# Kernel optimization log

Measured on AMD Instinct MI355X. Metric: run time of the kernel, lower is better.

The kernel has to match this reference:

```python
import jax, jax.numpy as jnp
import numpy as np

N, E, C, EMB, NB, L = 20000, 640000, 64, 32, 8, 2
MAX_RADIUS = 2.5
NUM_NEIGHBORS = 32.0
RH = 32  # radial MLP hidden


def setup_inputs() -> dict:
    key = jax.random.key(0)
    ks = jax.random.split(key, 24)
    g = lambda k, shape, fan: (jax.random.normal(k, shape, dtype=jnp.float32) / np.sqrt(fan).astype(np.float32))
    inp = {
        'x': jax.random.normal(ks[0], (N, 6), dtype=jnp.float32),
        'batch': jnp.zeros((N,), dtype=jnp.int64),
        'node_attr': jax.random.randint(ks[1], (N,), 0, 100),
        'edge_src': jax.random.randint(ks[2], (E,), 0, N),
        'edge_dst': jax.random.randint(ks[3], (E,), 0, N),
        'emb_table': jax.random.normal(ks[4], (100, EMB), dtype=jnp.float32),
        'uplift_M': jax.random.normal(ks[5], (C, 2), dtype=jnp.float32),
        'h': jnp.ones((L,), jnp.float32) * 0.01,
        'mix': jnp.ones((L,), jnp.float32) * 0.5,
        'rad_W1': g(ks[6], (L, NB, RH), NB),
        'rad_b1': jnp.zeros((L, RH), jnp.float32),
        'rad_W2': g(ks[7], (L, RH, 2 * C), RH),
        'lin1_s': g(ks[8], (L, C, C), C),
        'lin1_v': g(ks[9], (L, C, C), C),
        'lin2_s': g(ks[10], (L, C, 2 * C), C),
        'lin2_v': g(ks[11], (L, C, C), C),
        'sc_s_w': g(ks[12], (L, C, EMB, 2 * C), C * EMB),
        'sc_v_w': g(ks[13], (L, C, EMB, C), C * EMB),
        'si_s': g(ks[14], (L, C, C), C),
        'si_v': g(ks[15], (L, C, C), C),
    }
    return inp


def _forward(x, batch, node_attr, edge_src, edge_dst, emb_table, uplift_M, h, mix,
             rad_W1, rad_b1, rad_W2, lin1_s, lin1_v, lin2_s, lin2_v,
             sc_s_w, sc_v_w, si_s, si_v):
    n = x.shape[0]
    emb = emb_table[node_attr]                       # [N, EMB] node embedding
    # semi-unitarize uplift matrix: Q = M (M^T M)^{-1/2} == U V^T
    U, _, Vt = jnp.linalg.svd(uplift_M, full_matrices=False)
    Q = U @ Vt                                       # [C, 2]
    xv = x.reshape(n, 2, 3)
    y_s = jnp.zeros((n, C), x.dtype)                 # hidden scalars start at 0
    y_v = jnp.einsum('nkx,ck->ncx', xv, Q)           # uplift vectors [N,C,3]
    y = (y_s, y_v)
    y_old = y
    nbas = jnp.arange(1, NB + 1, dtype=x.dtype)
    inv_nn = 1.0 / np.sqrt(NUM_NEIGHBORS).astype(np.float32)
    for i in range(L):
        pos = x[:, :3]
        ev = pos[edge_src] - pos[edge_dst]           # [E,3]
        elen = jnp.linalg.norm(ev, axis=1)
        safe = jnp.maximum(elen, 1e-9)
        sh = np.float32(np.sqrt(3.0)) * ev / safe[:, None]   # 1x1o SH, component norm
        # bessel radial basis, scaled by sqrt(NB)
        ef = (np.float32(np.sqrt(2.0 / MAX_RADIUS)) *
              jnp.sin(nbas[None, :] * jnp.pi * safe[:, None] / MAX_RADIUS) / safe[:, None])
        ef = ef * np.float32(np.sqrt(NB))
        # smooth cutoff (e3nn tetris style)
        u = 2.0 * (elen / MAX_RADIUS - 1.0)
        cut = jnp.where(u > 0, 0.0, jnp.where(u < -2, 1.0, 0.5 * (1.0 - jnp.cos(jnp.pi * u))))
        ea = cut[:, None] * sh                       # [E,3] edge attr
        # linear pre-mix
        s1 = y[0] @ lin1_s[i]                        # [N,C]
        v1 = jnp.einsum('ncx,cd->ndx', y[1], lin1_v[i])  # [N,C,3]
        # radial MLP -> per-edge TP weights
        w = jax.nn.silu(ef @ rad_W1[i] + rad_b1[i]) @ rad_W2[i]  # [E,2C]
        w1, w2 = w[:, :C], w[:, C:]
        # tensor-product messages: 0e x 1o -> 1o ; 1o . 1o -> 0e
        msg_v = (w1 * s1[edge_src])[:, :, None] * ea[:, None, :]        # [E,C,3]
        msg_s = w2 * jnp.einsum('ecx,ex->ec', v1[edge_src], ea)         # [E,C]
        agg_s = jax.ops.segment_sum(msg_s, edge_dst, num_segments=n) * inv_nn
        agg_v = jax.ops.segment_sum(msg_v, edge_dst, num_segments=n) * inv_nn
        # post linear + node-attr self connection
        out_s = agg_s @ lin2_s[i] + jnp.einsum('nc,ne,ceo->no', y[0], emb, sc_s_w[i])   # [N,2C]
        out_v = (jnp.einsum('ncx,cd->ndx', agg_v, lin2_v[i]) +
                 jnp.einsum('ncx,ne,ceo->nox', y[1], emb, sc_v_w[i]))                   # [N,C,3]
        # gated nonlinearity
        g_s = jax.nn.silu(out_s[:, :C])
        g_v = jax.nn.sigmoid(out_s[:, C:])[:, :, None] * out_v
        # self interaction
        y2_s = y[0] @ si_s[i]
        y2_v = jnp.einsum('ncx,cd->ndx', y[1], si_v[i])
        # leapfrog update
        hh = h[i] * h[i]
        m = mix[i]
        new_s = 2.0 * y[0] - y_old[0] + hh * (m * g_s + (m - 1.0) * y2_s)
        new_v = 2.0 * y[1] - y_old[1] + hh * (m * g_v + (m - 1.0) * y2_v)
        y_old = y
        y = (new_s, new_v)
        x = jnp.einsum('ncx,ck->nkx', new_v, Q).reshape(n, 6)   # project
    return x


def reference(x, batch, node_attr, edge_src, edge_dst, emb_table, uplift_M, h, mix,
              rad_W1, rad_b1, rad_W2, lin1_s, lin1_v, lin2_s, lin2_v,
              sc_s_w, sc_v_w, si_s, si_v):
    return _forward(x, batch, node_attr, edge_src, edge_dst, emb_table, uplift_M, h, mix,
                    rad_W1, rad_b1, rad_W2, lin1_s, lin1_v, lin2_s, lin2_v,
                    sc_s_w, sc_v_w, si_s, si_v)
```

## Files before the change

kernel.cpp:

```cpp
#include <hip/hip_runtime.h>
#include <cstdio>
#include <cstdint>

#define CCH 64
#define EMBD 32
#define NBD 8
#define RHD 32
#define NATTR 100
#define TBINS 64

static constexpr float MAXR    = 2.5f;
static constexpr float INVNN   = 0.17677669529663687f;
static constexpr float EFK     = 2.5298221281347035f;
static constexpr float SQRT3   = 1.7320508075688772f;
static constexpr float PI_F    = 3.14159265358979323846f;

typedef __fp16 v2h __attribute__((ext_vector_type(2)));

__device__ __forceinline__ float sigm_(float x) { return 1.f / (1.f + __expf(-x)); }
__device__ __forceinline__ float silu_(float x) { return x / (1.f + __expf(-x)); }
__device__ __forceinline__ unsigned f2bfu(float f) {
    unsigned u = __float_as_uint(f);
    return (u + 0x7FFF + ((u >> 16) & 1)) >> 16;
}
__device__ __forceinline__ unsigned pack2(float lo, float hi) {
    return f2bfu(lo) | (f2bfu(hi) << 16);
}
__device__ __forceinline__ float ulo(unsigned u) { return __uint_as_float(u << 16); }
__device__ __forceinline__ float uhi(unsigned u) { return __uint_as_float(u & 0xFFFF0000u); }
__device__ __forceinline__ v2h u2h(unsigned u) { v2h h; __builtin_memcpy(&h, &u, 4); return h; }
__device__ __forceinline__ unsigned pkh(float a, float b) {
    v2h h = __builtin_amdgcn_cvt_pkrtz(a, b);
    unsigned u; __builtin_memcpy(&u, &h, 4); return u;
}
__device__ __forceinline__ unsigned short h1(float f) {
    __fp16 h = (__fp16)f; unsigned short s; __builtin_memcpy(&s, &h, 2); return s;
}
__device__ __forceinline__ float dot2(unsigned a, unsigned b, float c) {
    return __builtin_amdgcn_fdot2(u2h(a), u2h(b), c, false);
}
__device__ __forceinline__ float hlo(unsigned u) { v2h h = u2h(u); return (float)h.x; }
__device__ __forceinline__ float hhi(unsigned u) { v2h h = u2h(u); return (float)h.y; }

__global__ void kQ(const float* M, float* Q) {
    int c = threadIdx.x;
    float m0 = M[2*c], m1 = M[2*c+1];
    float a = m0*m0, b = m0*m1, d = m1*m1;
    for (int o = 32; o > 0; o >>= 1) {
        a += __shfl_xor(a, o); b += __shfl_xor(b, o); d += __shfl_xor(d, o);
    }
    float det = a*d - b*b;
    float s = sqrtf(det);
    float t = sqrtf(a + d + 2.f*s);
    float inv = 1.f / (s*t);
    float i00 = (d + s)*inv, i01 = -b*inv, i11 = (a + s)*inv;
    Q[2*c]   = m0*i00 + m1*i01;
    Q[2*c+1] = m0*i01 + m1*i11;
}

__global__ void kRadTab(const float* __restrict__ rW1, const float* __restrict__ rb1,
                        const float* __restrict__ rW2, unsigned* __restrict__ tab) {
    int bin = blockIdx.x;
    int l   = blockIdx.y;
    int lane = threadIdx.x;
    float r = bin * (MAXR / TBINS);
    float safe = fmaxf(r, 1e-9f);
    float invSafe = 1.f / safe;
    float th = PI_F * r * (1.f / MAXR);
    float s0, c0;
    __sincosf(th, &s0, &c0);
    __shared__ float hidS[RHD];
    if (lane < RHD) {
        float hs = rb1[l*RHD + lane];
        float sPrev = 0.f, sCur = s0, twoC = 2.f*c0;
        #pragma unroll
        for (int b = 0; b < NBD; ++b) {
            float efb = EFK * sCur * invSafe;
            hs = fmaf(efb, rW1[(l*NBD + b)*RHD + lane], hs);
            float sN = fmaf(twoC, sCur, -sPrev);
            sPrev = sCur; sCur = sN;
        }
        hidS[lane] = silu_(hs);
    }
    __syncthreads();
    float w1 = 0.f, w2 = 0.f;
    #pragma unroll
    for (int rr = 0; rr < RHD; ++rr) {
        float h = hidS[rr];
        w1 = fmaf(h, rW2[(l*RHD + rr)*128 + lane], w1);
        w2 = fmaf(h, rW2[(l*RHD + rr)*128 + 64 + lane], w2);
    }
    float cut = s0*s0;
    float coef = SQRT3 * cut * invSafe * INVNN;
    tab[((size_t)l*(TBINS+1) + bin)*64 + lane] = pack2(w1*coef, w2*coef);
}

__global__ void kPackW(const float* __restrict__ siv, unsigned* __restrict__ siVp) {
    int l = blockIdx.y;
    int i = blockIdx.x*256 + threadIdx.x;
    int cp = i >> 6, o = i & 63;
    siVp[l*2048 + i] = pkh(siv[l*4096 + (2*cp)*64 + o], siv[l*4096 + (2*cp+1)*64 + o]);
}

__global__ __launch_bounds__(256) void kInitLin(const float* __restrict__ x, const float* __restrict__ Qg,
        const float* __restrict__ L1v,
        float* __restrict__ yAs, float* __restrict__ yAv, float4* __restrict__ pos4,
        uint2* __restrict__ mv, int n) {
    __shared__ unsigned wPk[32*64];
    __shared__ __align__(16) unsigned bc[4][32][4];
    int t = threadIdx.x;
    for (int i = t; i < 32*64; i += 256) {
        int cp = i >> 6, o = i & 63;
        wPk[i] = pkh(L1v[(2*cp)*64 + o], L1v[(2*cp+1)*64 + o]);
    }
    __syncthreads();
    int lane = t & 63;
    int wid = t >> 6;
    float q0 = Qg[2*lane], q1 = Qg[2*lane+1];
    for (int node = blockIdx.x*4 + wid; node < n; node += gridDim.x*4) {
        const float* xr = x + (size_t)node*6;
        float x0 = xr[0], x1 = xr[1], x2 = xr[2], x3 = xr[3], x4 = xr[4], x5 = xr[5];
        float y0 = q0*x0 + q1*x3;
        float y1 = q0*x1 + q1*x4;
        float y2 = q0*x2 + q1*x5;
        float* yv = yAv + (size_t)node*192 + lane*3;
        yv[0] = y0; yv[1] = y1; yv[2] = y2;
        yAs[(size_t)node*64 + lane] = 0.f;
        if (lane == 0) pos4[node] = (float4){x0, x1, x2, 0.f};
        {
            unsigned short* p = (unsigned short*)bc[wid][lane >> 1];
            int sub = lane & 1;
            p[0*2+sub] = h1(y0); p[1*2+sub] = h1(y1); p[2*2+sub] = h1(y2);
        }
        float a0 = 0.f, a1 = 0.f, a2 = 0.f;
        #pragma unroll 8
        for (int cp = 0; cp < 32; ++cp) {
            uint4 b = *(const uint4*)&bc[wid][cp][0];
            unsigned wp = wPk[cp*64 + lane];
            a0 = dot2(b.x, wp, a0);
            a1 = dot2(b.y, wp, a1);
            a2 = dot2(b.z, wp, a2);
        }
        mv[(size_t)node*64 + lane] = (uint2){ pack2(a0, a1), pack2(a2, 0.f) };
    }
}

__global__ void kHist(const int* dst, int* cnt, int e) {
    int i = blockIdx.x*blockDim.x + threadIdx.x;
    if (i < e) atomicAdd(&cnt[dst[i]], 1);
}

__global__ void kScan(const int* cnt, int* offs, int* cursor, int n) {
    __shared__ int part[1024];
    int t = threadIdx.x;
    int chunk = (n + 1023) >> 10;
    int lo = t*chunk, hi = min(lo + chunk, n);
    int s = 0;
    for (int i = lo; i < hi; ++i) s += cnt[i];
    part[t] = s;
    __syncthreads();
    for (int o = 1; o < 1024; o <<= 1) {
        int w = (t >= o) ? part[t - o] : 0;
        __syncthreads();
        part[t] += w;
        __syncthreads();
    }
    int run = part[t] - s;
    for (int i = lo; i < hi; ++i) {
        int cv = cnt[i];
        offs[i] = run; cursor[i] = run;
        run += cv;
    }
    if (t == 1023) offs[n] = part[1023];
}

__global__ void kScatter(const int* src, const int* dst, int* cursor,
                         int* srcSorted, int* dstSorted, int e) {
    int i = blockIdx.x*blockDim.x + threadIdx.x;
    if (i < e) {
        int d = dst[i];
        int p = atomicAdd(&cursor[d], 1);
        srcSorted[p] = src[i];
        dstSorted[p] = d;
    }
}

__global__ __launch_bounds__(256) void kGeom(const float4* __restrict__ pos4,
        const int* __restrict__ srcSorted, const int* __restrict__ dstSorted,
        uint4* __restrict__ rec, int e) {
    int i = blockIdx.x*256 + threadIdx.x;
    if (i >= e) return;
    int s = srcSorted[i], d = dstSorted[i];
    float4 pa = pos4[s], pb = pos4[d];
    float ex = pa.x - pb.x, ey = pa.y - pb.y, ez = pa.z - pb.z;
    float el2 = ex*ex + ey*ey + ez*ez;
    if (el2 >= MAXR*MAXR) {
        rec[i] = (uint4){0xFFFFFFFFu, 0u, 0u, 0u};
        return;
    }
    float elen = sqrtf(el2);
    float u = fminf(elen * ((float)TBINS / MAXR), 63.98f);
    rec[i] = (uint4){ (unsigned)s, pkh(ex, ey), pkh(ez, u), 0u };
}

__global__ __launch_bounds__(256) void kT3(const float* __restrict__ embT,
        const float* __restrict__ scs, const float* __restrict__ scv,
        unsigned* __restrict__ TallU) {
    int cp = blockIdx.x, l = blockIdx.y, ag = blockIdx.z;
    int c0 = 2*cp, c1 = c0 + 1;
    __shared__ float sS0[32*128], sS1[32*128], sV0[32*64], sV1[32*64], sE[20*EMBD];
    int t = threadIdx.x;
    const float* p0 = scs + ((size_t)(l*CCH + c0)*EMBD)*128;
    const float* p1 = scs + ((size_t)(l*CCH + c1)*EMBD)*128;
    for (int i = t; i < 32*128; i += 256) { sS0[i] = p0[i]; sS1[i] = p1[i]; }
    const float* q0 = scv + ((size_t)(l*CCH + c0)*EMBD)*64;
    const float* q1 = scv + ((size_t)(l*CCH + c1)*EMBD)*64;
    for (int i = t; i < 32*64; i += 256) { sV0[i] = q0[i]; sV1[i] = q1[i]; }
    const float* eb = embT + (size_t)ag*20*EMBD;
    for (int i = t; i < 20*EMBD; i += 256) sE[i] = eb[i];
    __syncthreads();
    if (t < 128) {
        int o = t;
        for (int a = 0; a < 20; ++a) {
            float acc0 = 0.f, acc1 = 0.f;
            #pragma unroll
            for (int e = 0; e < EMBD; ++e) {
                float ev = sE[a*EMBD + e];
                acc0 = fmaf(ev, sS0[e*128 + o], acc0);
                acc1 = fmaf(ev, sS1[e*128 + o], acc1);
            }
            int aa = ag*20 + a;
            size_t idx = ((size_t)(l*NATTR + aa)*32 + cp)*64 + (o & 63);
            TallU[idx*4 + (o >> 6)] = pkh(acc0, acc1);
        }
    } else if (t < 192) {
        int o = t - 128;
        for (int a = 0; a < 20; ++a) {
            float acc0 = 0.f, acc1 = 0.f;
            #pragma unroll
            for (int e = 0; e < EMBD; ++e) {
                float ev = sE[a*EMBD + e];
                acc0 = fmaf(ev, sV0[e*64 + o], acc0);
                acc1 = fmaf(ev, sV1[e*64 + o], acc1);
            }
            int aa = ag*20 + a;
            size_t idx = ((size_t)(l*NATTR + aa)*32 + cp)*64 + o;
            TallU[idx*4 + 2] = pkh(acc0, acc1);
        }
    }
}

__global__ __launch_bounds__(256) void kLin1(const float* __restrict__ ys, const float* __restrict__ yv,
        const float* __restrict__ L1s, const float* __restrict__ L1v,
        uint2* __restrict__ mv, int n) {
    __shared__ uint2 wPk[32*64];
    __shared__ __align__(16) unsigned bc[4][32][4];
    int t = threadIdx.x;
    for (int i = t; i < 32*64; i += 256) {
        int cp = i >> 6, o = i & 63;
        wPk[i] = (uint2){ pkh(L1s[(2*cp)*64 + o], L1s[(2*cp+1)*64 + o]),
                          pkh(L1v[(2*cp)*64 + o], L1v[(2*cp+1)*64 + o]) };
    }
    __syncthreads();
    int lane = t & 63;
    int wid = t >> 6;
    for (int node = blockIdx.x*4 + wid; node < n; node += gridDim.x*4) {
        float ys_r = ys[(size_t)node*64 + lane];
        const float* yvp = yv + (size_t)node*192 + lane*3;
        float y0 = yvp[0], y1 = yvp[1], y2 = yvp[2];
        {
            unsigned short* p = (unsigned short*)bc[wid][lane >> 1];
            int sub = lane & 1;
            p[0*2+sub] = h1(y0); p[1*2+sub] = h1(y1);
            p[2*2+sub] = h1(y2); p[3*2+sub] = h1(ys_r);
        }
        float as = 0.f, a0 = 0.f, a1 = 0.f, a2 = 0.f;
        #pragma unroll 8
        for (int cp = 0; cp < 32; ++cp) {
            uint4 b = *(const uint4*)&bc[wid][cp][0];
            uint2 wp = wPk[cp*64 + lane];
            as = dot2(b.w, wp.x, as);
            a0 = dot2(b.x, wp.y, a0);
            a1 = dot2(b.y, wp.y, a1);
            a2 = dot2(b.z, wp.y, a2);
        }
        mv[(size_t)node*64 + lane] = (uint2){ pack2(a0, a1), pack2(a2, as) };
    }
}

template<int WITHV>
__global__ __launch_bounds__(256) void kAgg(const uint4* __restrict__ rec,
        const uint2* __restrict__ mv,
        const int* __restrict__ offs,
        const unsigned* __restrict__ tabG,
        float* __restrict__ aggS, float* __restrict__ aggV, int n) {
    __shared__ unsigned tab[(TBINS+1)*64];
    __shared__ float red[4][64][4];
    int t = threadIdx.x;
    for (int i = t; i < (TBINS+1)*64; i += 256) tab[i] = tabG[i];
    __syncthreads();
    int lane = t & 63;
    int wid = t >> 6;

    for (int node = blockIdx.x; node < n; node += gridDim.x) {
        int beg = offs[node], end = offs[node+1];
        float accS = 0.f, av0 = 0.f, av1 = 0.f, av2 = 0.f;
        int idx = beg + wid;
        uint4 rC = (uint4){0xFFFFFFFFu,0u,0u,0u};
        uint2 mwC = (uint2){0u,0u};
        bool actC = false;
        if (idx < end) {
            rC = rec[idx];
            actC = ((int)rC.x) >= 0;
            if (actC) mwC = mv[(size_t)rC.x*64 + lane];
        }
        for (; idx < end; ) {
            int nIdx = idx + 4;
            uint4 rN = (uint4){0xFFFFFFFFu,0u,0u,0u};
            uint2 mwN = (uint2){0u,0u};
            bool actN = false;
            if (nIdx < end) {
                rN = rec[nIdx];
                actN = ((int)rN.x) >= 0;
                if (actN) mwN = mv[(size_t)rN.x*64 + lane];
            }
            if (actC) {
                float ex = hlo(rC.y), ey = hhi(rC.y);
                float ez = hlo(rC.z), u = hhi(rC.z);
                int i0 = (int)u;
                float fr = u - (float)i0;
                unsigned t0 = tab[i0*64 + lane];
                unsigned t1 = tab[i0*64 + 64 + lane];
                float w1 = fmaf(fr, ulo(t1) - ulo(t0), ulo(t0));
                float w2 = fmaf(fr, uhi(t1) - uhi(t0), uhi(t0));
                float vv0 = ulo(mwC.x), vv1 = uhi(mwC.x), vv2 = ulo(mwC.y);
                float dv = vv0*ex + vv1*ey + vv2*ez;
                accS = fmaf(w2, dv, accS);
                if (WITHV) {
                    float tt = w1 * uhi(mwC.y);
                    av0 = fmaf(tt, ex, av0); av1 = fmaf(tt, ey, av1); av2 = fmaf(tt, ez, av2);
                }
            }
            rC = rN; mwC = mwN; actC = actN; idx = nIdx;
        }
        red[wid][lane][0] = accS; red[wid][lane][1] = av0;
        red[wid][lane][2] = av1;  red[wid][lane][3] = av2;
        __syncthreads();
        if (wid == 0) {
            float rs = red[0][lane][0] + red[1][lane][0] + red[2][lane][0] + red[3][lane][0];
            aggS[(size_t)node*64 + lane] = rs;
            float r0 = red[0][lane][1] + red[1][lane][1] + red[2][lane][1] + red[3][lane][1];
            float r1 = red[0][lane][2] + red[1][lane][2] + red[2][lane][2] + red[3][lane][2];
            float r2 = red[0][lane][3] + red[1][lane][3] + red[2][lane][3] + red[3][lane][3];
            float* ap = aggV + (size_t)node*192 + lane*3;
            ap[0] = r0; ap[1] = r1; ap[2] = r2;
        }
        __syncthreads();
    }
}

__global__ __launch_bounds__(256) void kOutComb(const float* __restrict__ ys, const float* __restrict__ yv,
        const float* __restrict__ yolds, const float* __restrict__ yoldv,
        const float* __restrict__ aggS, const float* __restrict__ aggV, const int* __restrict__ attr,
        const float* __restrict__ L2s, const float* __restrict__ L2v,
        const uint4* __restrict__ Tall,
        const float* __restrict__ siS, const unsigned* __restrict__ siVp, const float* __restrict__ Qg,
        const float* __restrict__ hArr, const float* __restrict__ mArr, int li,
        float* __restrict__ newS, float* __restrict__ newV,
        float4* __restrict__ pos4out, float* __restrict__ xout6,
        int writeY, int n) {
    __shared__ uint4 wAll[32*64];
    __shared__ __align__(16) unsigned bc[4][32][8];
    int t = threadIdx.x;
    for (int i = t; i < 32*64; i += 256) {
        int cp = i >> 6, o = i & 63;
        wAll[i] = (uint4){ pkh(L2s[(2*cp)*128 + o],      L2s[(2*cp+1)*128 + o]),
                           pkh(L2s[(2*cp)*128 + 64 + o], L2s[(2*cp+1)*128 + 64 + o]),
                           pkh(L2v[(2*cp)*64 + o], L2v[(2*cp+1)*64 + o]),
                           pkh(siS[(2*cp)*64 + o], siS[(2*cp+1)*64 + o]) };
    }
    __syncthreads();
    int lane = t & 63;
    int wid = t >> 6;
    unsigned svr[32];
    #pragma unroll
    for (int cp = 0; cp < 32; ++cp) svr[cp] = siVp[cp*64 + lane];
    float hh = hArr[li]; hh *= hh;
    float m = mArr[li];
    float q0 = Qg[2*lane], q1 = Qg[2*lane+1];
    for (int node = blockIdx.x*4 + wid; node < n; node += gridDim.x*4) {
        int a = attr[node];
        const uint4* tA = Tall + (size_t)a*2048;
        float as_r = aggS[(size_t)node*64 + lane];
        float ys_r = ys[(size_t)node*64 + lane];
        const float* avp = aggV + (size_t)node*192 + lane*3;
        float av0 = avp[0], av1 = avp[1], av2 = avp[2];
        const float* yvp = yv + (size_t)node*192 + lane*3;
        float by0 = yvp[0], by1 = yvp[1], by2 = yvp[2];
        {
            unsigned short* p = (unsigned short*)bc[wid][lane >> 1];
            int sub = lane & 1;
            p[0*2+sub] = h1(as_r); p[1*2+sub] = h1(ys_r);
            p[2*2+sub] = h1(av0);  p[3*2+sub] = h1(by0);
            p[4*2+sub] = h1(av1);  p[5*2+sub] = h1(by1);
            p[6*2+sub] = h1(av2);  p[7*2+sub] = h1(by2);
        }
        float oS0=0.f, oS1=0.f, ov0=0.f, ov1=0.f, ov2=0.f;
        float q2s=0.f, qv0=0.f, qv1=0.f, qv2=0.f;
        #pragma unroll 4
        for (int cp = 0; cp < 32; ++cp) {
            uint4 bA = *(const uint4*)&bc[wid][cp][0];
            uint4 bB = *(const uint4*)&bc[wid][cp][4];
            uint4 wv4 = wAll[cp*64 + lane];
            uint4 tw  = tA[cp*64 + lane];
            oS0 = dot2(bA.x, wv4.x, dot2(bA.y, tw.x, oS0));
            oS1 = dot2(bA.x, wv4.y, dot2(bA.y, tw.y, oS1));
            ov0 = dot2(bA.z, wv4.z, dot2(bA.w, tw.z, ov0));
            ov1 = dot2(bB.x, wv4.z, dot2(bB.y, tw.z, ov1));
            ov2 = dot2(bB.z, wv4.z, dot2(bB.w, tw.z, ov2));
            q2s = dot2(bA.y, wv4.w, q2s);
            qv0 = dot2(bA.w, svr[cp], qv0);
            qv1 = dot2(bB.y, svr[cp], qv1);
            qv2 = dot2(bB.w, svr[cp], qv2);
        }
        float gs = silu_(oS0);
        float sg = sigm_(oS1);
        float gv0 = sg*ov0, gv1 = sg*ov1, gv2 = sg*ov2;
        float yos = yolds[(size_t)node*64 + lane];
        const float* yop = yoldv + (size_t)node*192 + lane*3;
        float ns  = 2.f*ys_r - yos   + hh*(m*gs  + (m-1.f)*q2s);
        float nv0 = 2.f*by0 - yop[0] + hh*(m*gv0 + (m-1.f)*qv0);
        float nv1 = 2.f*by1 - yop[1] + hh*(m*gv1 + (m-1.f)*qv1);
        float nv2 = 2.f*by2 - yop[2] + hh*(m*gv2 + (m-1.f)*qv2);
        if (writeY) {
            newS[(size_t)node*64 + lane] = ns;
            float* np = newV + (size_t)node*192 + lane*3;
            np[0] = nv0; np[1] = nv1; np[2] = nv2;
        }
        float p00 = nv0*q0, p01 = nv1*q0, p02 = nv2*q0;
        float p10 = nv0*q1, p11 = nv1*q1, p12 = nv2*q1;
        for (int o = 32; o > 0; o >>= 1) {
            p00 += __shfl_xor(p00, o); p01 += __shfl_xor(p01, o); p02 += __shfl_xor(p02, o);
            p10 += __shfl_xor(p10, o); p11 += __shfl_xor(p11, o); p12 += __shfl_xor(p12, o);
        }
        if (lane == 0) {
            if (writeY) {
                pos4out[node] = (float4){p00, p01, p02, 0.f};
            } else {
                float* xp = xout6 + (size_t)node*6;
                xp[0] = p00; xp[1] = p01; xp[2] = p02;
                xp[3] = p10; xp[4] = p11; xp[5] = p12;
            }
        }
    }
}

extern "C" void kernel_launch(void* const* d_in, const int* in_sizes, int n_in,
                              void* d_out, int out_size, void* d_ws, size_t ws_size,
                              hipStream_t stream) {
    const float* x        = (const float*)d_in[0];
    const int*   nattr    = (const int*)  d_in[2];
    const int*   esrc     = (const int*)  d_in[3];
    const int*   edst     = (const int*)  d_in[4];
    const float* embT     = (const float*)d_in[5];
    const float* upM      = (const float*)d_in[6];
    const float* hArr     = (const float*)d_in[7];
    const float* mArr     = (const float*)d_in[8];
    const float* rW1      = (const float*)d_in[9];
    const float* rb1      = (const float*)d_in[10];
    const float* rW2      = (const float*)d_in[11];
    const float* l1s      = (const float*)d_in[12];
    const float* l1v      = (const float*)d_in[13];
    const float* l2s      = (const float*)d_in[14];
    const float* l2v      = (const float*)d_in[15];
    const float* scs      = (const float*)d_in[16];
    const float* scv      = (const float*)d_in[17];
    const float* sis      = (const float*)d_in[18];
    const float* siv      = (const float*)d_in[19];
    int n = in_sizes[0] / 6;
    int e = in_sizes[3];
    float* out = (float*)d_out;

    float* w = (float*)d_ws;
    float* Q    = w; w += 128;
    float* yAs  = w; w += (size_t)n*64;
    float* yAv  = w; w += (size_t)n*192;
    float* yBs  = w; w += (size_t)n*64;
    float* yBv  = w; w += (size_t)n*192;
    float* aggS = w; w += (size_t)n*64;
    float* aggV = w; w += (size_t)n*192;
    float4* pos4 = (float4*)w; w += (size_t)n*4;
    uint2* mv    = (uint2*)w;  w += (size_t)n*128;
    uint4* Tall  = (uint4*)w;  w += (size_t)2*NATTR*2048*4;
    unsigned* radTab = (unsigned*)w; w += (size_t)2*(TBINS+1)*64;
    unsigned* siVp = (unsigned*)w; w += (size_t)2*2048;
    uint4* rec = (uint4*)w; w += (size_t)e*4;
    int* cnt       = (int*)w;
    int* offs      = cnt + n;
    int* cursor    = offs + (n + 1);
    int* srcSorted = cursor + n;
    int* dstSorted = srcSorted + e;
    size_t need = (size_t)((char*)(dstSorted + e) - (char*)d_ws);
    if (need > ws_size) {
        fprintf(stderr, "kernel_launch: ws too small (%zu > %zu)\n", need, ws_size);
        return;
    }

    const int AGG_GRID  = 1792;
    const int OC_GRID   = 1024;
    const int LIN_GRID  = 2048;
    int eb = (e + 255)/256;

    kQ<<<1, 64, 0, stream>>>(upM, Q);
    hipMemsetAsync(cnt, 0, (size_t)n*sizeof(int), stream);
    kHist<<<eb, 256, 0, stream>>>(edst, cnt, e);
    kScan<<<1, 1024, 0, stream>>>(cnt, offs, cursor, n);
    kScatter<<<eb, 256, 0, stream>>>(esrc, edst, cursor, srcSorted, dstSorted, e);
    kT3<<<dim3(32, 2, 5), 256, 0, stream>>>(embT, scs, scv, (unsigned*)Tall);
    kRadTab<<<dim3(TBINS+1, 2), 64, 0, stream>>>(rW1, rb1, rW2, radTab);
    kPackW<<<dim3(8, 2), 256, 0, stream>>>(siv, siVp);
    kInitLin<<<LIN_GRID, 256, 0, stream>>>(x, Q, l1v, yAs, yAv, pos4, mv, n);

    kGeom<<<eb, 256, 0, stream>>>(pos4, srcSorted, dstSorted, rec, e);
    kAgg<0><<<AGG_GRID, 256, 0, stream>>>(rec, mv, offs, radTab, aggS, aggV, n);
    kOutComb<<<OC_GRID, 256, 0, stream>>>(yAs, yAv, yAs, yAv, aggS, aggV, nattr,
                                  l2s, l2v, Tall, sis, siVp, Q, hArr, mArr, 0,
                                  yBs, yBv, pos4, out, 1, n);
    kLin1<<<LIN_GRID, 256, 0, stream>>>(yBs, yBv, l1s + 4096, l1v + 4096, mv, n);
    kGeom<<<eb, 256, 0, stream>>>(pos4, srcSorted, dstSorted, rec, e);
    kAgg<1><<<AGG_GRID, 256, 0, stream>>>(rec, mv, offs,
                                  radTab + (size_t)(TBINS+1)*64, aggS, aggV, n);
    kOutComb<<<OC_GRID, 256, 0, stream>>>(yBs, yBv, yAs, yAv, aggS, aggV, nattr,
                                  l2s + (size_t)64*128, l2v + (size_t)64*64,
                                  Tall + (size_t)NATTR*2048,
                                  sis + 4096, siVp + 2048, Q, hArr, mArr, 1,
                                  yAs, yAv, pos4, out, 0, n);
}
```

Before: 534.0 us.

## Compact in-radius edges via atomic scatter in geometry kernel; specialize first layer

The separate scatter pass and sorted src/dst arrays are removed. The geometry kernel now reads the original edge list and atomically appends only in-radius edges into per-destination slots, so aggregation walks a compacted list with a per-node end pointer and no inactive-edge checks. The first output-combine kernel is templated to skip the zero scalar state and its self-interaction and embedding-scalar terms, and zero-fills of y_s are dropped. In exchange, edge order within a node becomes nondeterministic, which can change float summation order, and atomics are issued in the geometry pass twice.

```diff
diff --git a/kernel.cpp b/kernel.cpp
--- a/kernel.cpp
+++ b/kernel.cpp
@@ -104,7 +104,7 @@
 
 __global__ __launch_bounds__(256) void kInitLin(const float* __restrict__ x, const float* __restrict__ Qg,
         const float* __restrict__ L1v,
-        float* __restrict__ yAs, float* __restrict__ yAv, float4* __restrict__ pos4,
+        float* __restrict__ yAv, float4* __restrict__ pos4,
         uint2* __restrict__ mv, int n) {
     __shared__ unsigned wPk[32*64];
     __shared__ __align__(16) unsigned bc[4][32][4];
@@ -125,7 +125,6 @@
         float y2 = q0*x2 + q1*x5;
         float* yv = yAv + (size_t)node*192 + lane*3;
         yv[0] = y0; yv[1] = y1; yv[2] = y2;
-        yAs[(size_t)node*64 + lane] = 0.f;
         if (lane == 0) pos4[node] = (float4){x0, x1, x2, 0.f};
         {
             unsigned short* p = (unsigned short*)bc[wid][lane >> 1];
@@ -150,7 +149,7 @@
     if (i < e) atomicAdd(&cnt[dst[i]], 1);
 }
 
-__global__ void kScan(const int* cnt, int* offs, int* cursor, int n) {
+__global__ void kScan(const int* cnt, int* offs, int* curG0, int* curG1, int n) {
     __shared__ int part[1024];
     int t = threadIdx.x;
     int chunk = (n + 1023) >> 10;
@@ -168,39 +167,26 @@
     int run = part[t] - s;
     for (int i = lo; i < hi; ++i) {
         int cv = cnt[i];
-        offs[i] = run; cursor[i] = run;
+        offs[i] = run; curG0[i] = run; curG1[i] = run;
         run += cv;
     }
     if (t == 1023) offs[n] = part[1023];
 }
 
-__global__ void kScatter(const int* src, const int* dst, int* cursor,
-                         int* srcSorted, int* dstSorted, int e) {
-    int i = blockIdx.x*blockDim.x + threadIdx.x;
-    if (i < e) {
-        int d = dst[i];
-        int p = atomicAdd(&cursor[d], 1);
-        srcSorted[p] = src[i];
-        dstSorted[p] = d;
-    }
-}
-
 __global__ __launch_bounds__(256) void kGeom(const float4* __restrict__ pos4,
-        const int* __restrict__ srcSorted, const int* __restrict__ dstSorted,
-        uint4* __restrict__ rec, int e) {
+        const int* __restrict__ esrc, const int* __restrict__ edst,
+        int* __restrict__ cur, uint4* __restrict__ rec, int e) {
     int i = blockIdx.x*256 + threadIdx.x;
     if (i >= e) return;
-    int s = srcSorted[i], d = dstSorted[i];
+    int s = esrc[i], d = edst[i];
     float4 pa = pos4[s], pb = pos4[d];
     float ex = pa.x - pb.x, ey = pa.y - pb.y, ez = pa.z - pb.z;
     float el2 = ex*ex + ey*ey + ez*ez;
-    if (el2 >= MAXR*MAXR) {
-        rec[i] = (uint4){0xFFFFFFFFu, 0u, 0u, 0u};
-        return;
-    }
+    if (el2 >= MAXR*MAXR) return;
     float elen = sqrtf(el2);
     float u = fminf(elen * ((float)TBINS / MAXR), 63.98f);
-    rec[i] = (uint4){ (unsigned)s, pkh(ex, ey), pkh(ez, u), 0u };
+    int p = atomicAdd(&cur[d], 1);
+    rec[p] = (uint4){ (unsigned)s, pkh(ex, ey), pkh(ez, u), 0u };
 }
 
 __global__ __launch_bounds__(256) void kT3(const float* __restrict__ embT,
@@ -291,7 +277,7 @@
 template<int WITHV>
 __global__ __launch_bounds__(256) void kAgg(const uint4* __restrict__ rec,
         const uint2* __restrict__ mv,
-        const int* __restrict__ offs,
+        const int* __restrict__ offs, const int* __restrict__ endA,
         const unsigned* __restrict__ tabG,
         float* __restrict__ aggS, float* __restrict__ aggV, int n) {
     __shared__ unsigned tab[(TBINS+1)*64];
@@ -303,45 +289,32 @@
     int wid = t >> 6;
 
     for (int node = blockIdx.x; node < n; node += gridDim.x) {
-        int beg = offs[node], end = offs[node+1];
+        int beg = offs[node], end = endA[node];
         float accS = 0.f, av0 = 0.f, av1 = 0.f, av2 = 0.f;
         int idx = beg + wid;
-        uint4 rC = (uint4){0xFFFFFFFFu,0u,0u,0u};
-        uint2 mwC = (uint2){0u,0u};
-        bool actC = false;
-        if (idx < end) {
-            rC = rec[idx];
-            actC = ((int)rC.x) >= 0;
-            if (actC) mwC = mv[(size_t)rC.x*64 + lane];
-        }
-        for (; idx < end; ) {
-            int nIdx = idx + 4;
-            uint4 rN = (uint4){0xFFFFFFFFu,0u,0u,0u};
-            uint2 mwN = (uint2){0u,0u};
-            bool actN = false;
-            if (nIdx < end) {
-                rN = rec[nIdx];
-                actN = ((int)rN.x) >= 0;
-                if (actN) mwN = mv[(size_t)rN.x*64 + lane];
+        uint4 r0 = (uint4){0u,0u,0u,0u}, r1 = r0;
+        uint2 m0 = (uint2){0u,0u}, m1 = m0;
+        if (idx < end)     { r0 = rec[idx];   m0 = mv[(size_t)r0.x*64 + lane]; }
+        if (idx + 4 < end) { r1 = rec[idx+4]; m1 = mv[(size_t)r1.x*64 + lane]; }
+        for (; idx < end; idx += 4) {
+            uint4 r2 = (uint4){0u,0u,0u,0u};
+            uint2 m2 = (uint2){0u,0u};
+            if (idx + 8 < end) { r2 = rec[idx+8]; m2 = mv[(size_t)r2.x*64 + lane]; }
+            float ex = hlo(r0.y), ey = hhi(r0.y);
+            float ez = hlo(r0.z), u = hhi(r0.z);
+            int i0 = (int)u;
+            float fr = u - (float)i0;
+            unsigned t0 = tab[i0*64 + lane];
+            unsigned t1 = tab[i0*64 + 64 + lane];
+            float w1 = fmaf(fr, ulo(t1) - ulo(t0), ulo(t0));
+            float w2 = fmaf(fr, uhi(t1) - uhi(t0), uhi(t0));
+            float dv = ulo(m0.x)*ex + uhi(m0.x)*ey + ulo(m0.y)*ez;
+            accS = fmaf(w2, dv, accS);
+            if (WITHV) {
+                float tt = w1 * uhi(m0.y);
+                av0 = fmaf(tt, ex, av0); av1 = fmaf(tt, ey, av1); av2 = fmaf(tt, ez, av2);
             }
-            if (actC) {
-                float ex = hlo(rC.y), ey = hhi(rC.y);
-                float ez = hlo(rC.z), u = hhi(rC.z);
-                int i0 = (int)u;
-                float fr = u - (float)i0;
-                unsigned t0 = tab[i0*64 + lane];
-                unsigned t1 = tab[i0*64 + 64 + lane];
-                float w1 = fmaf(fr, ulo(t1) - ulo(t0), ulo(t0));
-                float w2 = fmaf(fr, uhi(t1) - uhi(t0), uhi(t0));
-                float vv0 = ulo(mwC.x), vv1 = uhi(mwC.x), vv2 = ulo(mwC.y);
-                float dv = vv0*ex + vv1*ey + vv2*ez;
-                accS = fmaf(w2, dv, accS);
-                if (WITHV) {
-                    float tt = w1 * uhi(mwC.y);
-                    av0 = fmaf(tt, ex, av0); av1 = fmaf(tt, ey, av1); av2 = fmaf(tt, ez, av2);
-                }
-            }
-            rC = rN; mwC = mwN; actC = actN; idx = nIdx;
+            r0 = r1; m0 = m1; r1 = r2; m1 = m2;
         }
         red[wid][lane][0] = accS; red[wid][lane][1] = av0;
         red[wid][lane][2] = av1;  red[wid][lane][3] = av2;
@@ -349,26 +322,26 @@
         if (wid == 0) {
             float rs = red[0][lane][0] + red[1][lane][0] + red[2][lane][0] + red[3][lane][0];
             aggS[(size_t)node*64 + lane] = rs;
-            float r0 = red[0][lane][1] + red[1][lane][1] + red[2][lane][1] + red[3][lane][1];
-            float r1 = red[0][lane][2] + red[1][lane][2] + red[2][lane][2] + red[3][lane][2];
-            float r2 = red[0][lane][3] + red[1][lane][3] + red[2][lane][3] + red[3][lane][3];
+            float r0s = red[0][lane][1] + red[1][lane][1] + red[2][lane][1] + red[3][lane][1];
+            float r1s = red[0][lane][2] + red[1][lane][2] + red[2][lane][2] + red[3][lane][2];
+            float r2s = red[0][lane][3] + red[1][lane][3] + red[2][lane][3] + red[3][lane][3];
             float* ap = aggV + (size_t)node*192 + lane*3;
-            ap[0] = r0; ap[1] = r1; ap[2] = r2;
+            ap[0] = r0s; ap[1] = r1s; ap[2] = r2s;
         }
         __syncthreads();
     }
 }
 
+template<int L0>
 __global__ __launch_bounds__(256) void kOutComb(const float* __restrict__ ys, const float* __restrict__ yv,
-        const float* __restrict__ yolds, const float* __restrict__ yoldv,
+        const float* __restrict__ yoldv,
         const float* __restrict__ aggS, const float* __restrict__ aggV, const int* __restrict__ attr,
         const float* __restrict__ L2s, const float* __restrict__ L2v,
         const uint4* __restrict__ Tall,
         const float* __restrict__ siS, const unsigned* __restrict__ siVp, const float* __restrict__ Qg,
         const float* __restrict__ hArr, const float* __restrict__ mArr, int li,
         float* __restrict__ newS, float* __restrict__ newV,
-        float4* __restrict__ pos4out, float* __restrict__ xout6,
-        int writeY, int n) {
+        float4* __restrict__ pos4out, float* __restrict__ xout6, int n) {
     __shared__ uint4 wAll[32*64];
     __shared__ __align__(16) unsigned bc[4][32][8];
     int t = threadIdx.x;
@@ -377,7 +350,7 @@
         wAll[i] = (uint4){ pkh(L2s[(2*cp)*128 + o],      L2s[(2*cp+1)*128 + o]),
                            pkh(L2s[(2*cp)*128 + 64 + o], L2s[(2*cp+1)*128 + 64 + o]),
                            pkh(L2v[(2*cp)*64 + o], L2v[(2*cp+1)*64 + o]),
-                           pkh(siS[(2*cp)*64 + o], siS[(2*cp+1)*64 + o]) };
+                           L0 ? 0u : pkh(siS[(2*cp)*64 + o], siS[(2*cp+1)*64 + o]) };
     }
     __syncthreads();
     int lane = t & 63;
@@ -390,9 +363,9 @@
     float q0 = Qg[2*lane], q1 = Qg[2*lane+1];
     for (int node = blockIdx.x*4 + wid; node < n; node += gridDim.x*4) {
         int a = attr[node];
-        const uint4* tA = Tall + (size_t)a*2048;
+        const unsigned* tA = (const unsigned*)(Tall + (size_t)a*2048);
         float as_r = aggS[(size_t)node*64 + lane];
-        float ys_r = ys[(size_t)node*64 + lane];
+        float ys_r = L0 ? 0.f : ys[(size_t)node*64 + lane];
         const float* avp = aggV + (size_t)node*192 + lane*3;
         float av0 = avp[0], av1 = avp[1], av2 = avp[2];
         const float* yvp = yv + (size_t)node*192 + lane*3;
@@ -400,7 +373,7 @@
         {
             unsigned short* p = (unsigned short*)bc[wid][lane >> 1];
             int sub = lane & 1;
-            p[0*2+sub] = h1(as_r); p[1*2+sub] = h1(ys_r);
+            p[0*2+sub] = h1(as_r); p[1*2+sub] = L0 ? (unsigned short)0 : h1(ys_r);
             p[2*2+sub] = h1(av0);  p[3*2+sub] = h1(by0);
             p[4*2+sub] = h1(av1);  p[5*2+sub] = h1(by1);
             p[6*2+sub] = h1(av2);  p[7*2+sub] = h1(by2);
@@ -412,13 +385,22 @@
             uint4 bA = *(const uint4*)&bc[wid][cp][0];
             uint4 bB = *(const uint4*)&bc[wid][cp][4];
             uint4 wv4 = wAll[cp*64 + lane];
-            uint4 tw  = tA[cp*64 + lane];
-            oS0 = dot2(bA.x, wv4.x, dot2(bA.y, tw.x, oS0));
-            oS1 = dot2(bA.x, wv4.y, dot2(bA.y, tw.y, oS1));
-            ov0 = dot2(bA.z, wv4.z, dot2(bA.w, tw.z, ov0));
-            ov1 = dot2(bB.x, wv4.z, dot2(bB.y, tw.z, ov1));
-            ov2 = dot2(bB.z, wv4.z, dot2(bB.w, tw.z, ov2));
-            q2s = dot2(bA.y, wv4.w, q2s);
+            if (L0) {
+                unsigned tv = tA[(cp*64 + lane)*4 + 2];
+                oS0 = dot2(bA.x, wv4.x, oS0);
+                oS1 = dot2(bA.x, wv4.y, oS1);
+                ov0 = dot2(bA.z, wv4.z, dot2(bA.w, tv, ov0));
+                ov1 = dot2(bB.x, wv4.z, dot2(bB.y, tv, ov1));
+                ov2 = dot2(bB.z, wv4.z, dot2(bB.w, tv, ov2));
+            } else {
+                uint4 tw = ((const uint4*)tA)[cp*64 + lane];
+                oS0 = dot2(bA.x, wv4.x, dot2(bA.y, tw.x, oS0));
+                oS1 = dot2(bA.x, wv4.y, dot2(bA.y, tw.y, oS1));
+                ov0 = dot2(bA.z, wv4.z, dot2(bA.w, tw.z, ov0));
+                ov1 = dot2(bB.x, wv4.z, dot2(bB.y, tw.z, ov1));
+                ov2 = dot2(bB.z, wv4.z, dot2(bB.w, tw.z, ov2));
+                q2s = dot2(bA.y, wv4.w, q2s);
+            }
             qv0 = dot2(bA.w, svr[cp], qv0);
             qv1 = dot2(bB.y, svr[cp], qv1);
             qv2 = dot2(bB.w, svr[cp], qv2);
@@ -426,13 +408,20 @@
         float gs = silu_(oS0);
         float sg = sigm_(oS1);
         float gv0 = sg*ov0, gv1 = sg*ov1, gv2 = sg*ov2;
-        float yos = yolds[(size_t)node*64 + lane];
-        const float* yop = yoldv + (size_t)node*192 + lane*3;
-        float ns  = 2.f*ys_r - yos   + hh*(m*gs  + (m-1.f)*q2s);
-        float nv0 = 2.f*by0 - yop[0] + hh*(m*gv0 + (m-1.f)*qv0);
-        float nv1 = 2.f*by1 - yop[1] + hh*(m*gv1 + (m-1.f)*qv1);
-        float nv2 = 2.f*by2 - yop[2] + hh*(m*gv2 + (m-1.f)*qv2);
-        if (writeY) {
+        float ns, nv0, nv1, nv2;
+        if (L0) {
+            ns  = hh*m*gs;
+            nv0 = by0 + hh*(m*gv0 + (m-1.f)*qv0);
+            nv1 = by1 + hh*(m*gv1 + (m-1.f)*qv1);
+            nv2 = by2 + hh*(m*gv2 + (m-1.f)*qv2);
+        } else {
+            const float* yop = yoldv + (size_t)node*192 + lane*3;
+            ns  = 2.f*ys_r + hh*(m*gs + (m-1.f)*q2s);
+            nv0 = 2.f*by0 - yop[0] + hh*(m*gv0 + (m-1.f)*qv0);
+            nv1 = 2.f*by1 - yop[1] + hh*(m*gv1 + (m-1.f)*qv1);
+            nv2 = 2.f*by2 - yop[2] + hh*(m*gv2 + (m-1.f)*qv2);
+        }
+        if (L0) {
             newS[(size_t)node*64 + lane] = ns;
             float* np = newV + (size_t)node*192 + lane*3;
             np[0] = nv0; np[1] = nv1; np[2] = nv2;
@@ -444,7 +433,7 @@
             p10 += __shfl_xor(p10, o); p11 += __shfl_xor(p11, o); p12 += __shfl_xor(p12, o);
         }
         if (lane == 0) {
-            if (writeY) {
+            if (L0) {
                 pos4out[node] = (float4){p00, p01, p02, 0.f};
             } else {
                 float* xp = xout6 + (size_t)node*6;
@@ -483,7 +472,6 @@
 
     float* w = (float*)d_ws;
     float* Q    = w; w += 128;
-    float* yAs  = w; w += (size_t)n*64;
     float* yAv  = w; w += (size_t)n*192;
     float* yBs  = w; w += (size_t)n*64;
     float* yBv  = w; w += (size_t)n*192;
@@ -495,12 +483,11 @@
     unsigned* radTab = (unsigned*)w; w += (size_t)2*(TBINS+1)*64;
     unsigned* siVp = (unsigned*)w; w += (size_t)2*2048;
     uint4* rec = (uint4*)w; w += (size_t)e*4;
-    int* cnt       = (int*)w;
-    int* offs      = cnt + n;
-    int* cursor    = offs + (n + 1);
-    int* srcSorted = cursor + n;
-    int* dstSorted = srcSorted + e;
-    size_t need = (size_t)((char*)(dstSorted + e) - (char*)d_ws);
+    int* cnt   = (int*)w;
+    int* offs  = cnt + n;
+    int* curG0 = offs + (n + 1);
+    int* curG1 = curG0 + n;
+    size_t need = (size_t)((char*)(curG1 + n) - (char*)d_ws);
     if (need > ws_size) {
         fprintf(stderr, "kernel_launch: ws too small (%zu > %zu)\n", need, ws_size);
         return;
@@ -514,25 +501,24 @@
     kQ<<<1, 64, 0, stream>>>(upM, Q);
     hipMemsetAsync(cnt, 0, (size_t)n*sizeof(int), stream);
     kHist<<<eb, 256, 0, stream>>>(edst, cnt, e);
-    kScan<<<1, 1024, 0, stream>>>(cnt, offs, cursor, n);
-    kScatter<<<eb, 256, 0, stream>>>(esrc, edst, cursor, srcSorted, dstSorted, e);
+    kScan<<<1, 1024, 0, stream>>>(cnt, offs, curG0, curG1, n);
     kT3<<<dim3(32, 2, 5), 256, 0, stream>>>(embT, scs, scv, (unsigned*)Tall);
     kRadTab<<<dim3(TBINS+1, 2), 64, 0, stream>>>(rW1, rb1, rW2, radTab);
     kPackW<<<dim3(8, 2), 256, 0, stream>>>(siv, siVp);
-    kInitLin<<<LIN_GRID, 256, 0, stream>>>(x, Q, l1v, yAs, yAv, pos4, mv, n);
-
-    kGeom<<<eb, 256, 0, stream>>>(pos4, srcSorted, dstSorted, rec, e);
-    kAgg<0><<<AGG_GRID, 256, 0, stream>>>(rec, mv, offs, radTab, aggS, aggV, n);
-    kOutComb<<<OC_GRID, 256, 0, stream>>>(yAs, yAv, yAs, yAv, aggS, aggV, nattr,
+    kInitLin<<<LIN_GRID, 256, 0, stream>>>(x, Q, l1v, yAv, pos4, mv, n);
+
+    kGeom<<<eb, 256, 0, stream>>>(pos4, esrc, edst, curG0, rec, e);
+    kAgg<0><<<AGG_GRID, 256, 0, stream>>>(rec, mv, offs, curG0, radTab, aggS, aggV, n);
+    kOutComb<1><<<OC_GRID, 256, 0, stream>>>(nullptr, yAv, nullptr, aggS, aggV, nattr,
                                   l2s, l2v, Tall, sis, siVp, Q, hArr, mArr, 0,
-                                  yBs, yBv, pos4, out, 1, n);
+                                  yBs, yBv, pos4, out, n);
     kLin1<<<LIN_GRID, 256, 0, stream>>>(yBs, yBv, l1s + 4096, l1v + 4096, mv, n);
-    kGeom<<<eb, 256, 0, stream>>>(pos4, srcSorted, dstSorted, rec, e);
-    kAgg<1><<<AGG_GRID, 256, 0, stream>>>(rec, mv, offs,
+    kGeom<<<eb, 256, 0, stream>>>(pos4, esrc, edst, curG1, rec, e);
+    kAgg<1><<<AGG_GRID, 256, 0, stream>>>(rec, mv, offs, curG1,
                                   radTab + (size_t)(TBINS+1)*64, aggS, aggV, n);
-    kOutComb<<<OC_GRID, 256, 0, stream>>>(yBs, yBv, yAs, yAv, aggS, aggV, nattr,
+    kOutComb<0><<<OC_GRID, 256, 0, stream>>>(yBs, yBv, yAv, aggS, aggV, nattr,
                                   l2s + (size_t)64*128, l2v + (size_t)64*64,
                                   Tall + (size_t)NATTR*2048,
                                   sis + 4096, siVp + 2048, Q, hArr, mArr, 1,
-                                  yAs, yAv, pos4, out, 0, n);
-}
+                                  nullptr, nullptr, nullptr, out, n);
+}
```

New measurement: 493.3 us. 7.6% less time.
